# Kernel tuning notes

Hardware: AMD Instinct MI355X
Metric: run time of the kernel (lower is better)

## Reference

```python
import jax, jax.numpy as jnp
import numpy as np

VOCAB, D, H, L, SEQ = 32000, 768, 12, 6, 1024
HD = D // H
DFF = 4 * D
EPS = 1e-5


def _ln(x, g, b):
    mu = jnp.mean(x, axis=-1, keepdims=True)
    var = jnp.var(x, axis=-1, keepdims=True)
    return (x - mu) * jax.lax.rsqrt(var + EPS) * g + b


def setup_inputs() -> dict:
    key = jax.random.key(0)
    ks = jax.random.split(key, 10)
    s = lambda *sh: 0.02
    return {
        "idx": jax.random.randint(ks[0], (2, SEQ), 0, VOCAB, dtype=jnp.int64) if jax.config.jax_enable_x64 else jax.random.randint(ks[0], (2, SEQ), 0, VOCAB, dtype=jnp.int32),
        "tok_emb": jax.random.normal(ks[1], (VOCAB, D), jnp.float32) * 0.02,
        "pos_emb": jax.random.normal(ks[2], (SEQ, D), jnp.float32) * 0.02,
        "Wqkv": jax.random.normal(ks[3], (L, D, 3 * D), jnp.float32) * 0.02,
        "bqkv": jnp.zeros((L, 3 * D), jnp.float32),
        "Wo": jax.random.normal(ks[4], (L, D, D), jnp.float32) * 0.02,
        "bo": jnp.zeros((L, D), jnp.float32),
        "ln1_g": jnp.ones((L, D), jnp.float32),
        "ln1_b": jnp.zeros((L, D), jnp.float32),
        "ln2_g": jnp.ones((L, D), jnp.float32),
        "ln2_b": jnp.zeros((L, D), jnp.float32),
        "W1": jax.random.normal(ks[5], (L, D, DFF), jnp.float32) * 0.02,
        "b1": jnp.zeros((L, DFF), jnp.float32),
        "W2": jax.random.normal(ks[6], (L, DFF, D), jnp.float32) * 0.02,
        "b2": jnp.zeros((L, D), jnp.float32),
        "lnf_g": jnp.ones((D,), jnp.float32),
        "lnf_b": jnp.zeros((D,), jnp.float32),
        "Wlm": jax.random.normal(ks[7], (D, VOCAB), jnp.float32) * 0.02,
    }


def _forward(idx, tok_emb, pos_emb, Wqkv, bqkv, Wo, bo, ln1_g, ln1_b,
             ln2_g, ln2_b, W1, b1, W2, b2, lnf_g, lnf_b, Wlm):
    B, T = idx.shape
    x = tok_emb[idx] + pos_emb[None, :T]  # [B,T,D]
    causal = jnp.tril(jnp.ones((T, T), bool))  # [T,T]
    for l in range(L):
        h = _ln(x, ln1_g[l], ln1_b[l])
        qkv = h @ Wqkv[l] + bqkv[l]  # [B,T,3D]
        qkv = qkv.reshape(B, T, 3, H, HD).transpose(2, 0, 3, 1, 4)
        q, k, v = qkv[0], qkv[1], qkv[2]  # each [B,H,T,HD]
        att = jnp.einsum('bhqd,bhkd->bhqk', q, k) / np.sqrt(HD).astype(np.float32)
        att = jnp.where(causal, att, -jnp.inf)
        att = jax.nn.softmax(att, axis=-1)
        o = jnp.einsum('bhqk,bhkd->bhqd', att, v)
        o = o.transpose(0, 2, 1, 3).reshape(B, T, D)
        x = x + o @ Wo[l] + bo[l]
        h = _ln(x, ln2_g[l], ln2_b[l])
        x = x + jax.nn.gelu(h @ W1[l] + b1[l], approximate=False) @ W2[l] + b2[l]
    x = _ln(x, lnf_g, lnf_b)
    return x @ Wlm  # [B,T,VOCAB]


def reference(idx, tok_emb, pos_emb, Wqkv, bqkv, Wo, bo, ln1_g, ln1_b,
              ln2_g, ln2_b, W1, b1, W2, b2, lnf_g, lnf_b, Wlm):
    return _forward(idx, tok_emb, pos_emb, Wqkv, bqkv, Wo, bo, ln1_g, ln1_b,
                    ln2_g, ln2_b, W1, b1, W2, b2, lnf_g, lnf_b, Wlm)
```

## Files before the change

kernel.cpp:

```cpp
#include <hip/hip_runtime.h>
#include <math.h>

#define TT   1024
#define DD   768
#define HH   12
#define LLAY 6
#define DFFN 3072
#define BB   2
#define NTOK (BB*TT)

typedef __bf16 bf16;
typedef __attribute__((ext_vector_type(8))) __bf16 bf16x8;
typedef __attribute__((ext_vector_type(4))) __bf16 bf16x4;
typedef __attribute__((ext_vector_type(4))) float f32x4;

__device__ inline unsigned pack_bf16x2(float a, float b) {
    union { bf16 h[2]; unsigned u; } un;
    un.h[0] = (bf16)a; un.h[1] = (bf16)b;
    return un.u;
}

__device__ inline void gload16(const bf16* g, bf16* l) {
    __builtin_amdgcn_global_load_lds((const void*)g, (void*)l, 16, 0, 0);
}

template<int N> __device__ inline void waitcnt_vm() {
    if constexpr (N == 0) asm volatile("s_waitcnt vmcnt(0)" ::: "memory");
    else if constexpr (N == 3) asm volatile("s_waitcnt vmcnt(3)" ::: "memory");
    else if constexpr (N == 4) asm volatile("s_waitcnt vmcnt(4)" ::: "memory");
}

__global__ __launch_bounds__(256) void embed_kernel(const int* __restrict__ idx,
                                                    const float* __restrict__ tok,
                                                    const float* __restrict__ pos,
                                                    float* __restrict__ x) {
    int bt = blockIdx.x;
    int t  = bt % TT;
    int id = idx[bt];
    const float* te = tok + (size_t)id * DD;
    const float* pe = pos + (size_t)t * DD;
    float* xr = x + (size_t)bt * DD;
    for (int d = threadIdx.x; d < DD; d += 256) xr[d] = te[d] + pe[d];
}

__global__ __launch_bounds__(256) void ln_kernel(const float* __restrict__ in,
                                                 const float* __restrict__ g,
                                                 const float* __restrict__ b,
                                                 bf16* __restrict__ out) {
    const int wid = threadIdx.x >> 6, lane = threadIdx.x & 63;
    const int row = blockIdx.x * 4 + wid;
    const float* xr = in + (size_t)row * DD;
    float4 v[3];
    float s = 0.f, s2 = 0.f;
#pragma unroll
    for (int j = 0; j < 3; ++j) {
        v[j] = *(const float4*)&xr[lane * 4 + 256 * j];
        s  += v[j].x + v[j].y + v[j].z + v[j].w;
        s2 += v[j].x * v[j].x + v[j].y * v[j].y + v[j].z * v[j].z + v[j].w * v[j].w;
    }
    for (int off = 32; off; off >>= 1) { s += __shfl_down(s, off); s2 += __shfl_down(s2, off); }
    s = __shfl(s, 0); s2 = __shfl(s2, 0);
    const float mu = s / (float)DD;
    const float rs = rsqrtf(s2 / (float)DD - mu * mu + 1e-5f);
    bf16* orow = out + (size_t)row * DD;
#pragma unroll
    for (int j = 0; j < 3; ++j) {
        float4 gg = *(const float4*)&g[lane * 4 + 256 * j];
        float4 bb = *(const float4*)&b[lane * 4 + 256 * j];
        bf16x4 o;
        o[0] = (bf16)((v[j].x - mu) * rs * gg.x + bb.x);
        o[1] = (bf16)((v[j].y - mu) * rs * gg.y + bb.y);
        o[2] = (bf16)((v[j].z - mu) * rs * gg.z + bb.z);
        o[3] = (bf16)((v[j].w - mu) * rs * gg.w + bb.w);
        *(bf16x4*)&orow[lane * 4 + 256 * j] = o;
    }
}

__device__ inline void convT_tile64(const float* __restrict__ in, bf16* __restrict__ out,
                                    int K, int N, int k0, int n0) {
    __shared__ float tile[64][65];
    const int c = threadIdx.x & 63, q = threadIdx.x >> 6;
#pragma unroll
    for (int i = 0; i < 16; ++i)
        tile[q + i * 4][c] = in[(size_t)(k0 + q + i * 4) * N + n0 + c];
    __syncthreads();
#pragma unroll
    for (int i = 0; i < 16; ++i)
        out[(size_t)(n0 + q + i * 4) * K + k0 + c] = (bf16)tile[c][q + i * 4];
}

__global__ __launch_bounds__(256) void convT_kernel(const float* __restrict__ in,
                                                    bf16* __restrict__ out,
                                                    int K, int N) {
    convT_tile64(in, out, K, N, blockIdx.y * 64, blockIdx.x * 64);
}

__global__ __launch_bounds__(256) void convT4_kernel(const float* __restrict__ w0,
                                                     const float* __restrict__ w1,
                                                     const float* __restrict__ w2,
                                                     const float* __restrict__ w3,
                                                     bf16* __restrict__ o0,
                                                     bf16* __restrict__ o1,
                                                     bf16* __restrict__ o2,
                                                     bf16* __restrict__ o3) {
    int bid = blockIdx.x;
    const float* in; bf16* out; int K, N, t;
    if (bid < 432)       { in = w0; out = o0; K = 768;  N = 2304; t = bid; }
    else if (bid < 576)  { in = w1; out = o1; K = 768;  N = 768;  t = bid - 432; }
    else if (bid < 1152) { in = w2; out = o2; K = 768;  N = 3072; t = bid - 576; }
    else                 { in = w3; out = o3; K = 3072; N = 768;  t = bid - 1152; }
    int nt = N / 64;
    convT_tile64(in, out, K, N, (t / nt) * 64, (t % nt) * 64);
}

template<int BM, int EPI>
__global__ __launch_bounds__(256) void mgemm(const bf16* __restrict__ A,
                                             const bf16* __restrict__ Bt,
                                             const float* __restrict__ bias,
                                             const float* __restrict__ res,
                                             void* __restrict__ Cout,
                                             bf16* __restrict__ vtout,
                                             int M, int N, int K) {
    constexpr int MF = BM / 32;
    constexpr int NF = 4;
    constexpr int AIT = BM / 64;
    constexpr int STG = AIT + 2;
    constexpr int ASZ = BM * 32;
    constexpr int BUFE = ASZ + 128 * 32;
    __shared__ __align__(16) bf16 smem[3 * BUFE];
    int bm = blockIdx.y * BM;
    int bn = blockIdx.x * 128;
    int tid = threadIdx.x;
    int lane = tid & 63;
    int w = tid >> 6;
    int wr = w >> 1, wc = w & 1;
    int l15 = lane & 15, g = lane >> 4;

    f32x4 acc[MF][NF];
#pragma unroll
    for (int m = 0; m < MF; ++m)
#pragma unroll
        for (int n = 0; n < NF; ++n) acc[m][n] = (f32x4){0.f, 0.f, 0.f, 0.f};

    int r = lane >> 2;
    int koff = ((lane & 3) ^ ((r >> 1) & 3)) * 8;
    const bf16* Ab = A + (size_t)(bm + w * 16 + r) * K + koff;
    const bf16* Bb = Bt + (size_t)(bn + w * 16 + r) * K + koff;

    auto stage = [&](int p, int k0) {
        bf16* base = smem + p * BUFE;
        bf16* Asb = base + w * 16 * 32;
        bf16* Bsb = base + ASZ + w * 16 * 32;
#pragma unroll
        for (int it = 0; it < AIT; ++it)
            gload16(Ab + (size_t)(it * 64) * K + k0, Asb + it * 64 * 32);
#pragma unroll
        for (int it = 0; it < 2; ++it)
            gload16(Bb + (size_t)(it * 64) * K + k0, Bsb + it * 64 * 32);
    };

    stage(0, 0);
    stage(1, 32);
    waitcnt_vm<STG>();
    __builtin_amdgcn_s_barrier();
    int cur = 0;

    for (int k0 = 0; k0 < K; k0 += 32) {
        const bf16* Ac = smem + cur * BUFE;
        const bf16* Bc = Ac + ASZ;
        bf16x8 af[MF], bfv[NF];
#pragma unroll
        for (int m = 0; m < MF; ++m) {
            int row = wr * (BM / 2) + m * 16 + l15;
            int gs = g ^ ((row >> 1) & 3);
            af[m] = *(const bf16x8*)&Ac[row * 32 + gs * 8];
        }
#pragma unroll
        for (int n = 0; n < NF; ++n) {
            int row = wc * 64 + n * 16 + l15;
            int gs = g ^ ((row >> 1) & 3);
            bfv[n] = *(const bf16x8*)&Bc[row * 32 + gs * 8];
        }
        bool st = (k0 + 64 < K);
        if (st) {
            int nxt = cur + 2; if (nxt >= 3) nxt -= 3;
            stage(nxt, k0 + 64);
        }
#pragma unroll
        for (int m = 0; m < MF; ++m)
#pragma unroll
            for (int n = 0; n < NF; ++n)
                acc[m][n] = __builtin_amdgcn_mfma_f32_16x16x32_bf16(af[m], bfv[n], acc[m][n], 0, 0, 0);
        if (st) waitcnt_vm<STG>();
        else    waitcnt_vm<0>();
        __builtin_amdgcn_s_barrier();
        cur = (cur == 2) ? 0 : cur + 1;
    }

    int lq = g * 4;
#pragma unroll
    for (int m = 0; m < MF; ++m) {
#pragma unroll
        for (int n = 0; n < NF; ++n) {
            int col = bn + wc * 64 + n * 16 + l15;
            float bv = bias[col];
            if (EPI == 4 && col >= 2 * DD) {
                int row0 = bm + wr * (BM / 2) + m * 16 + lq;
                int b = row0 >> 10, t0 = row0 & 1023;
                int hd = col - 2 * DD;
                union { bf16 h[4]; unsigned long long u; } pk;
#pragma unroll
                for (int j = 0; j < 4; ++j) pk.h[j] = (bf16)(acc[m][n][j] + bv);
                *(unsigned long long*)&vtout[((size_t)(b * DD + hd)) * TT + t0] = pk.u;
            } else {
#pragma unroll
                for (int j = 0; j < 4; ++j) {
                    int row = bm + wr * (BM / 2) + m * 16 + lq + j;
                    float v = acc[m][n][j] + bv;
                    if (EPI == 2) {
                        ((float*)Cout)[(size_t)row * N + col] = v + res[(size_t)row * N + col];
                    } else if (EPI == 3) {
                        v = 0.5f * v * (1.f + erff(v * 0.70710678118654752f));
                        ((bf16*)Cout)[(size_t)row * N + col] = (bf16)v;
                    } else if (EPI == 1) {
                        ((bf16*)Cout)[(size_t)row * N + col] = (bf16)v;
                    } else {
                        if (col < DD) v *= 0.125f;
                        ((bf16*)Cout)[(size_t)row * N + col] = (bf16)v;
                    }
                }
            }
        }
    }
}

__global__ __launch_bounds__(512, 2) void lmgemm(const bf16* __restrict__ A,
                                                 const bf16* __restrict__ Bt,
                                                 float* __restrict__ C) {
    constexpr int BUFE = 2 * 256 * 64;
    __shared__ __align__(16) bf16 smem[2 * BUFE];
    const int orig = blockIdx.x;
    const int xcd = orig & 7, local = orig >> 3;
    const int bnb = xcd * 16 + (local >> 3);
    if (bnb >= 125) return;
    const int bm = (local & 7) * 256;
    const int bn = bnb * 256;
    const int tid = threadIdx.x;
    const int w = tid >> 6, lane = tid & 63;
    const int wm = w >> 2, wn = w & 3;
    const int l15 = lane & 15, g = lane >> 4;

    const int swzr = (l15 >> 1) & 7;
    const int pc0 = (g ^ swzr) * 8;

    const int r8 = lane >> 3, c8 = lane & 7;
    const bf16* agp[4]; const bf16* bgp[4];
    int aldso[4], bldso[4];
#pragma unroll
    for (int j = 0; j < 4; ++j) {
        int br = w * 32 + j * 8 + r8;
        int swz = (br >> 1) & 7;
        agp[j] = A  + (size_t)(bm + br) * DD + (c8 ^ swz) * 8;
        bgp[j] = Bt + (size_t)(bn + br) * DD + (c8 ^ swz) * 8;
        aldso[j] = (w * 32 + j * 8) * 64;
        bldso[j] = 256 * 64 + (w * 32 + j * 8) * 64;
    }

    f32x4 acc[8][4];
#pragma unroll
    for (int m = 0; m < 8; ++m)
#pragma unroll
        for (int n = 0; n < 4; ++n) acc[m][n] = (f32x4){0.f, 0.f, 0.f, 0.f};

    {
        bf16* base = smem;
#pragma unroll
        for (int j = 0; j < 4; ++j) gload16(agp[j], base + aldso[j]);
#pragma unroll
        for (int j = 0; j < 4; ++j) gload16(bgp[j], base + bldso[j]);
    }
    __syncthreads();
    int cur = 0;

    for (int t = 0; t < 12; ++t) {
        const bf16* Ar = smem + cur * BUFE;
        const bf16* Br = Ar + 256 * 64;
        bf16* nbase = smem + (cur ^ 1) * BUFE;
        const int k0n = (t + 1) * 64;
        const bool st = (t < 11);
        if (st) {
#pragma unroll
            for (int j = 0; j < 4; ++j) gload16(agp[j] + k0n, nbase + aldso[j]);
        }
        bf16x8 af[8], bfv[4];
#pragma unroll
        for (int m = 0; m < 8; ++m)
            af[m] = *(const bf16x8*)&Ar[(wm * 128 + m * 16 + l15) * 64 + pc0];
#pragma unroll
        for (int n = 0; n < 4; ++n)
            bfv[n] = *(const bf16x8*)&Br[(wn * 64 + n * 16 + l15) * 64 + pc0];
        __builtin_amdgcn_s_setprio(1);
#pragma unroll
        for (int m = 0; m < 8; ++m)
#pragma unroll
            for (int n = 0; n < 4; ++n)
                acc[m][n] = __builtin_amdgcn_mfma_f32_16x16x32_bf16(af[m], bfv[n], acc[m][n], 0, 0, 0);
        __builtin_amdgcn_s_setprio(0);
        if (st) {
#pragma unroll
            for (int j = 0; j < 4; ++j) gload16(bgp[j] + k0n, nbase + bldso[j]);
        }
#pragma unroll
        for (int m = 0; m < 8; ++m)
            af[m] = *(const bf16x8*)&Ar[(wm * 128 + m * 16 + l15) * 64 + (pc0 ^ 32)];
#pragma unroll
        for (int n = 0; n < 4; ++n)
            bfv[n] = *(const bf16x8*)&Br[(wn * 64 + n * 16 + l15) * 64 + (pc0 ^ 32)];
        __builtin_amdgcn_s_setprio(1);
#pragma unroll
        for (int m = 0; m < 8; ++m)
#pragma unroll
            for (int n = 0; n < 4; ++n)
                acc[m][n] = __builtin_amdgcn_mfma_f32_16x16x32_bf16(af[m], bfv[n], acc[m][n], 0, 0, 0);
        __builtin_amdgcn_s_setprio(0);
        __syncthreads();
        cur ^= 1;
    }

    float* eb = (float*)smem + w * (16 * 68);
    const int rr = lane >> 2, c0 = (lane & 3) * 16;
#pragma unroll
    for (int mf = 0; mf < 8; ++mf) {
#pragma unroll
        for (int n = 0; n < 4; ++n)
#pragma unroll
            for (int j = 0; j < 4; ++j)
                eb[(g * 4 + j) * 68 + n * 16 + l15] = acc[mf][n][j];
        __syncthreads();
        const float* src = &eb[rr * 68 + c0];
        float* dst = C + (size_t)(bm + wm * 128 + mf * 16 + rr) * 32000 + bn + wn * 64 + c0;
        *(float4*)(dst + 0)  = *(const float4*)(src + 0);
        *(float4*)(dst + 4)  = *(const float4*)(src + 4);
        *(float4*)(dst + 8)  = *(const float4*)(src + 8);
        *(float4*)(dst + 12) = *(const float4*)(src + 12);
        __syncthreads();
    }
}

__global__ __launch_bounds__(256) void fattn_kernel(const bf16* __restrict__ qkv,
                                                    const bf16* __restrict__ vt,
                                                    bf16* __restrict__ o) {
    const int bh = blockIdx.y;
    const int b = bh / HH, h = bh % HH;
    const int qc = gridDim.x - 1 - blockIdx.x;
    const int q0 = qc * 64;
    const int tid = threadIdx.x;
    const int w = tid >> 6, lane = tid & 63;
    const int l15 = lane & 15, g = lane >> 4;

    __shared__ __align__(16) bf16 Ks[64 * 64];
    __shared__ __align__(16) bf16 Vs[64 * 64];
    __shared__ __align__(16) bf16 Ps[4][16 * 64];

    const size_t basebt = (size_t)b * TT;
    const int qw = q0 + w * 16;
    const int qg = qw + l15;

    bf16x8 bq0, bq1;
    {
        const bf16* qp = qkv + (basebt + qw + l15) * 2304 + h * 64 + g * 8;
        bq0 = *(const bf16x8*)(qp);
        bq1 = *(const bf16x8*)(qp + 32);
    }

    float mstate = -1e30f, lstate = 0.f;
    f32x4 oacc[4];
#pragma unroll
    for (int nf = 0; nf < 4; ++nf) oacc[nf] = (f32x4){0.f, 0.f, 0.f, 0.f};

    const int swzA = (l15 & 7) << 4;
    char* const psBase = (char*)&Ps[w][0];

    const int nchunk = qc + 1;
    for (int c = 0; c < nchunk; ++c) {
        const int kc = c * 64;
        __syncthreads();
        {
            int r0 = tid >> 3;
            int e0 = (tid & 7) * 8;
#pragma unroll
            for (int i = 0; i < 2; ++i) {
                int r = r0 + 32 * i;
                int swzW = (r & 7) << 4;
                bf16x8 kv = *(const bf16x8*)&qkv[(basebt + kc + r) * 2304 + DD + h * 64 + e0];
                *(bf16x8*)((char*)Ks + r * 128 + ((e0 * 2) ^ swzW)) = kv;
                bf16x8 vv = *(const bf16x8*)&vt[((size_t)bh * 64 + r) * TT + kc + e0];
                *(bf16x8*)((char*)Vs + r * 128 + ((e0 * 2) ^ swzW)) = vv;
            }
        }
        __syncthreads();
        if (kc > qw + 15) continue;

        f32x4 s[4];
        __builtin_amdgcn_s_setprio(1);
#pragma unroll
        for (int mf = 0; mf < 4; ++mf) {
            char* kr = (char*)Ks + (16 * mf + l15) * 128;
            bf16x8 ka0 = *(const bf16x8*)(kr + ((16 * g) ^ swzA));
            bf16x8 ka1 = *(const bf16x8*)(kr + ((64 + 16 * g) ^ swzA));
            f32x4 a = (f32x4){0.f, 0.f, 0.f, 0.f};
            a = __builtin_amdgcn_mfma_f32_16x16x32_bf16(ka0, bq0, a, 0, 0, 0);
            a = __builtin_amdgcn_mfma_f32_16x16x32_bf16(ka1, bq1, a, 0, 0, 0);
            s[mf] = a;
        }
        __builtin_amdgcn_s_setprio(0);
        if (kc + 63 > qw) {
#pragma unroll
            for (int mf = 0; mf < 4; ++mf)
#pragma unroll
                for (int j = 0; j < 4; ++j)
                    if (kc + 16 * mf + 4 * g + j > qg) s[mf][j] = -1e30f;
        }
        float cm = -1e30f;
#pragma unroll
        for (int mf = 0; mf < 4; ++mf)
#pragma unroll
            for (int j = 0; j < 4; ++j) cm = fmaxf(cm, s[mf][j]);
        cm = fmaxf(cm, __shfl_xor(cm, 16));
        cm = fmaxf(cm, __shfl_xor(cm, 32));
        float mnew = fmaxf(mstate, cm);
        float sc = __expf(mstate - mnew);
        mstate = mnew;
        float p[4][4];
        float psum = 0.f;
#pragma unroll
        for (int mf = 0; mf < 4; ++mf)
#pragma unroll
            for (int j = 0; j < 4; ++j) { float pv = __expf(s[mf][j] - mnew); p[mf][j] = pv; psum += pv; }
        psum += __shfl_xor(psum, 16);
        psum += __shfl_xor(psum, 32);
        lstate = lstate * sc + psum;
#pragma unroll
        for (int mf = 0; mf < 4; ++mf) {
            unsigned lo = pack_bf16x2(p[mf][0], p[mf][1]);
            unsigned hi = pack_bf16x2(p[mf][2], p[mf][3]);
            char* dst = psBase + l15 * 128 + ((32 * mf + 8 * g) ^ swzA);
            *(unsigned*)dst = lo;
            *(unsigned*)(dst + 4) = hi;
        }
        float s0 = __shfl(sc, 4 * g + 0), s1 = __shfl(sc, 4 * g + 1);
        float s2 = __shfl(sc, 4 * g + 2), s3 = __shfl(sc, 4 * g + 3);
#pragma unroll
        for (int nf = 0; nf < 4; ++nf) {
            oacc[nf][0] *= s0; oacc[nf][1] *= s1; oacc[nf][2] *= s2; oacc[nf][3] *= s3;
        }
        bf16x8 pa0 = *(const bf16x8*)(psBase + l15 * 128 + ((16 * g) ^ swzA));
        bf16x8 pa1 = *(const bf16x8*)(psBase + l15 * 128 + ((64 + 16 * g) ^ swzA));
        __builtin_amdgcn_s_setprio(1);
#pragma unroll
        for (int nf = 0; nf < 4; ++nf) {
            char* vr = (char*)Vs + (16 * nf + l15) * 128;
            bf16x8 vb0 = *(const bf16x8*)(vr + ((16 * g) ^ swzA));
            bf16x8 vb1 = *(const bf16x8*)(vr + ((64 + 16 * g) ^ swzA));
            oacc[nf] = __builtin_amdgcn_mfma_f32_16x16x32_bf16(pa0, vb0, oacc[nf], 0, 0, 0);
            oacc[nf] = __builtin_amdgcn_mfma_f32_16x16x32_bf16(pa1, vb1, oacc[nf], 0, 0, 0);
        }
        __builtin_amdgcn_s_setprio(0);
    }
    float linv = 1.f / lstate;
    float l0 = __shfl(linv, 4 * g + 0), l1 = __shfl(linv, 4 * g + 1);
    float l2 = __shfl(linv, 4 * g + 2), l3 = __shfl(linv, 4 * g + 3);
    float lj[4] = {l0, l1, l2, l3};
#pragma unroll
    for (int j = 0; j < 4; ++j) {
        bf16* orow = o + (size_t)(basebt + qw + 4 * g + j) * DD + h * 64 + l15;
#pragma unroll
        for (int nf = 0; nf < 4; ++nf)
            orow[16 * nf] = (bf16)(oacc[nf][j] * lj[j]);
    }
}

extern "C" void kernel_launch(void* const* d_in, const int* in_sizes, int n_in,
                              void* d_out, int out_size, void* d_ws, size_t ws_size,
                              hipStream_t stream) {
    (void)in_sizes; (void)n_in; (void)out_size; (void)ws_size;
    const int*   idx  = (const int*)d_in[0];
    const float* tok  = (const float*)d_in[1];
    const float* pos  = (const float*)d_in[2];
    const float* Wqkv = (const float*)d_in[3];
    const float* bqkv = (const float*)d_in[4];
    const float* Wo   = (const float*)d_in[5];
    const float* bo   = (const float*)d_in[6];
    const float* ln1g = (const float*)d_in[7];
    const float* ln1b = (const float*)d_in[8];
    const float* ln2g = (const float*)d_in[9];
    const float* ln2b = (const float*)d_in[10];
    const float* W1   = (const float*)d_in[11];
    const float* b1   = (const float*)d_in[12];
    const float* W2   = (const float*)d_in[13];
    const float* b2   = (const float*)d_in[14];
    const float* lnfg = (const float*)d_in[15];
    const float* lnfb = (const float*)d_in[16];
    const float* Wlm  = (const float*)d_in[17];
    float* out = (float*)d_out;

    char* ws = (char*)d_ws;
    float* x     = (float*)(ws);
    bf16*  abuf0 = (bf16*)(ws + 6291456);
    bf16*  abuf1 = (bf16*)(ws + 9437184);
    bf16*  qkvb  = (bf16*)(ws + 22020096);
    bf16*  vtb   = (bf16*)(ws + 31457280);
    bf16*  wbuf  = (bf16*)(ws + 34603008);

    bf16* wq = wbuf;
    bf16* wo = wbuf + 1769472;
    bf16* w1 = wbuf + 2359296;
    bf16* w2 = wbuf + 4718592;

    embed_kernel<<<NTOK, 256, 0, stream>>>(idx, tok, pos, x);

    for (int l = 0; l < LLAY; ++l) {
        convT4_kernel<<<1728, 256, 0, stream>>>(
            Wqkv + (size_t)l * DD * 3 * DD, Wo + (size_t)l * DD * DD,
            W1 + (size_t)l * DD * DFFN, W2 + (size_t)l * DFFN * DD,
            wq, wo, w1, w2);
        ln_kernel<<<NTOK / 4, 256, 0, stream>>>(x, ln1g + l * DD, ln1b + l * DD, abuf0);
        mgemm<128, 4><<<dim3(3 * DD / 128, NTOK / 128), 256, 0, stream>>>(
            abuf0, wq, bqkv + (size_t)l * 3 * DD, nullptr, qkvb, vtb, NTOK, 3 * DD, DD);
        fattn_kernel<<<dim3(TT / 64, BB * HH), 256, 0, stream>>>(qkvb, vtb, abuf0);
        mgemm<64, 2><<<dim3(DD / 128, NTOK / 64), 256, 0, stream>>>(
            abuf0, wo, bo + (size_t)l * DD, x, x, nullptr, NTOK, DD, DD);
        ln_kernel<<<NTOK / 4, 256, 0, stream>>>(x, ln2g + l * DD, ln2b + l * DD, abuf0);
        mgemm<128, 3><<<dim3(DFFN / 128, NTOK / 128), 256, 0, stream>>>(
            abuf0, w1, b1 + (size_t)l * DFFN, nullptr, abuf1, nullptr, NTOK, DFFN, DD);
        mgemm<64, 2><<<dim3(DD / 128, NTOK / 64), 256, 0, stream>>>(
            abuf1, w2, b2 + (size_t)l * DD, x, x, nullptr, NTOK, DD, DFFN);
    }
    ln_kernel<<<NTOK / 4, 256, 0, stream>>>(x, lnfg, lnfb, abuf0);
    convT_kernel<<<dim3(32000 / 64, DD / 64), 256, 0, stream>>>(Wlm, wbuf, DD, 32000);
    lmgemm<<<1024, 512, 0, stream>>>(abuf0, wbuf, out);
}
```

Baseline: 995.1 us.

## Prefetch K/V tiles into registers in attention; relax LM-head epilogue sync

The flash attention loop now loads the next K/V chunk from global memory into registers while the current chunk is computed, then writes it to shared memory at the top of the next iteration. This hides global load latency behind the MFMA and softmax work. Separately, the LM-head GEMM epilogue replaces its two block-wide barriers per fragment with a per-wave LDS wait and uses nontemporal float4 stores for the large logits output. This is safe because each wave uses its own staging region, and it cuts barrier stalls and cache pollution on the 256MB write, at the cost of some extra registers in the attention kernel.

New measurement: 1.271 ms. 27.8% more time.

```diff
diff --git a/kernel.cpp b/kernel.cpp
--- a/kernel.cpp
+++ b/kernel.cpp
@@ -336,14 +336,17 @@
 #pragma unroll
             for (int j = 0; j < 4; ++j)
                 eb[(g * 4 + j) * 68 + n * 16 + l15] = acc[mf][n][j];
-        __syncthreads();
+        asm volatile("s_waitcnt lgkmcnt(0)" ::: "memory");
         const float* src = &eb[rr * 68 + c0];
         float* dst = C + (size_t)(bm + wm * 128 + mf * 16 + rr) * 32000 + bn + wn * 64 + c0;
-        *(float4*)(dst + 0)  = *(const float4*)(src + 0);
-        *(float4*)(dst + 4)  = *(const float4*)(src + 4);
-        *(float4*)(dst + 8)  = *(const float4*)(src + 8);
-        *(float4*)(dst + 12) = *(const float4*)(src + 12);
-        __syncthreads();
+        f32x4 v0 = *(const f32x4*)(src + 0);
+        f32x4 v1 = *(const f32x4*)(src + 4);
+        f32x4 v2 = *(const f32x4*)(src + 8);
+        f32x4 v3 = *(const f32x4*)(src + 12);
+        __builtin_nontemporal_store(v0, (f32x4*)(dst + 0));
+        __builtin_nontemporal_store(v1, (f32x4*)(dst + 4));
+        __builtin_nontemporal_store(v2, (f32x4*)(dst + 8));
+        __builtin_nontemporal_store(v3, (f32x4*)(dst + 12));
     }
 }
 
@@ -381,91 +384,104 @@
     const int swzA = (l15 & 7) << 4;
     char* const psBase = (char*)&Ps[w][0];
 
+    const int r0 = tid >> 3;
+    const int e0 = (tid & 7) * 8;
+    bf16x8 kreg[2], vreg[2];
+#pragma unroll
+    for (int i = 0; i < 2; ++i) {
+        int r = r0 + 32 * i;
+        kreg[i] = *(const bf16x8*)&qkv[(basebt + r) * 2304 + DD + h * 64 + e0];
+        vreg[i] = *(const bf16x8*)&vt[((size_t)bh * 64 + r) * TT + e0];
+    }
+
     const int nchunk = qc + 1;
     for (int c = 0; c < nchunk; ++c) {
         const int kc = c * 64;
+#pragma unroll
+        for (int i = 0; i < 2; ++i) {
+            int r = r0 + 32 * i;
+            int swzW = (r & 7) << 4;
+            *(bf16x8*)((char*)Ks + r * 128 + ((e0 * 2) ^ swzW)) = kreg[i];
+            *(bf16x8*)((char*)Vs + r * 128 + ((e0 * 2) ^ swzW)) = vreg[i];
+        }
         __syncthreads();
-        {
-            int r0 = tid >> 3;
-            int e0 = (tid & 7) * 8;
+        if (c + 1 < nchunk) {
+            const int kc2 = kc + 64;
 #pragma unroll
             for (int i = 0; i < 2; ++i) {
                 int r = r0 + 32 * i;
-                int swzW = (r & 7) << 4;
-                bf16x8 kv = *(const bf16x8*)&qkv[(basebt + kc + r) * 2304 + DD + h * 64 + e0];
-                *(bf16x8*)((char*)Ks + r * 128 + ((e0 * 2) ^ swzW)) = kv;
-                bf16x8 vv = *(const bf16x8*)&vt[((size_t)bh * 64 + r) * TT + kc + e0];
-                *(bf16x8*)((char*)Vs + r * 128 + ((e0 * 2) ^ swzW)) = vv;
-            }
+                kreg[i] = *(const bf16x8*)&qkv[(basebt + kc2 + r) * 2304 + DD + h * 64 + e0];
+                vreg[i] = *(const bf16x8*)&vt[((size_t)bh * 64 + r) * TT + kc2 + e0];
+            }
+        }
+        if (kc <= qw + 15) {
+            f32x4 s[4];
+            __builtin_amdgcn_s_setprio(1);
+#pragma unroll
+            for (int mf = 0; mf < 4; ++mf) {
+                char* kr = (char*)Ks + (16 * mf + l15) * 128;
+                bf16x8 ka0 = *(const bf16x8*)(kr + ((16 * g) ^ swzA));
+                bf16x8 ka1 = *(const bf16x8*)(kr + ((64 + 16 * g) ^ swzA));
+                f32x4 a = (f32x4){0.f, 0.f, 0.f, 0.f};
+                a = __builtin_amdgcn_mfma_f32_16x16x32_bf16(ka0, bq0, a, 0, 0, 0);
+                a = __builtin_amdgcn_mfma_f32_16x16x32_bf16(ka1, bq1, a, 0, 0, 0);
+                s[mf] = a;
+            }
+            __builtin_amdgcn_s_setprio(0);
+            if (kc + 63 > qw) {
+#pragma unroll
+                for (int mf = 0; mf < 4; ++mf)
+#pragma unroll
+                    for (int j = 0; j < 4; ++j)
+                        if (kc + 16 * mf + 4 * g + j > qg) s[mf][j] = -1e30f;
+            }
+            float cm = -1e30f;
+#pragma unroll
+            for (int mf = 0; mf < 4; ++mf)
+#pragma unroll
+                for (int j = 0; j < 4; ++j) cm = fmaxf(cm, s[mf][j]);
+            cm = fmaxf(cm, __shfl_xor(cm, 16));
+            cm = fmaxf(cm, __shfl_xor(cm, 32));
+            float mnew = fmaxf(mstate, cm);
+            float sc = __expf(mstate - mnew);
+            mstate = mnew;
+            float p[4][4];
+            float psum = 0.f;
+#pragma unroll
+            for (int mf = 0; mf < 4; ++mf)
+#pragma unroll
+                for (int j = 0; j < 4; ++j) { float pv = __expf(s[mf][j] - mnew); p[mf][j] = pv; psum += pv; }
+            psum += __shfl_xor(psum, 16);
+            psum += __shfl_xor(psum, 32);
+            lstate = lstate * sc + psum;
+#pragma unroll
+            for (int mf = 0; mf < 4; ++mf) {
+                unsigned lo = pack_bf16x2(p[mf][0], p[mf][1]);
+                unsigned hi = pack_bf16x2(p[mf][2], p[mf][3]);
+                char* dst = psBase + l15 * 128 + ((32 * mf + 8 * g) ^ swzA);
+                *(unsigned*)dst = lo;
+                *(unsigned*)(dst + 4) = hi;
+            }
+            float s0 = __shfl(sc, 4 * g + 0), s1 = __shfl(sc, 4 * g + 1);
+            float s2 = __shfl(sc, 4 * g + 2), s3 = __shfl(sc, 4 * g + 3);
+#pragma unroll
+            for (int nf = 0; nf < 4; ++nf) {
+                oacc[nf][0] *= s0; oacc[nf][1] *= s1; oacc[nf][2] *= s2; oacc[nf][3] *= s3;
+            }
+            bf16x8 pa0 = *(const bf16x8*)(psBase + l15 * 128 + ((16 * g) ^ swzA));
+            bf16x8 pa1 = *(const bf16x8*)(psBase + l15 * 128 + ((64 + 16 * g) ^ swzA));
+            __builtin_amdgcn_s_setprio(1);
+#pragma unroll
+            for (int nf = 0; nf < 4; ++nf) {
+                char* vr = (char*)Vs + (16 * nf + l15) * 128;
+                bf16x8 vb0 = *(const bf16x8*)(vr + ((16 * g) ^ swzA));
+                bf16x8 vb1 = *(const bf16x8*)(vr + ((64 + 16 * g) ^ swzA));
+                oacc[nf] = __builtin_amdgcn_mfma_f32_16x16x32_bf16(pa0, vb0, oacc[nf], 0, 0, 0);
+                oacc[nf] = __builtin_amdgcn_mfma_f32_16x16x32_bf16(pa1, vb1, oacc[nf], 0, 0, 0);
+            }
+            __builtin_amdgcn_s_setprio(0);
         }
         __syncthreads();
-        if (kc > qw + 15) continue;
-
-        f32x4 s[4];
-        __builtin_amdgcn_s_setprio(1);
-#pragma unroll
-        for (int mf = 0; mf < 4; ++mf) {
-            char* kr = (char*)Ks + (16 * mf + l15) * 128;
-            bf16x8 ka0 = *(const bf16x8*)(kr + ((16 * g) ^ swzA));
-            bf16x8 ka1 = *(const bf16x8*)(kr + ((64 + 16 * g) ^ swzA));
-            f32x4 a = (f32x4){0.f, 0.f, 0.f, 0.f};
-            a = __builtin_amdgcn_mfma_f32_16x16x32_bf16(ka0, bq0, a, 0, 0, 0);
-            a = __builtin_amdgcn_mfma_f32_16x16x32_bf16(ka1, bq1, a, 0, 0, 0);
-            s[mf] = a;
-        }
-        __builtin_amdgcn_s_setprio(0);
-        if (kc + 63 > qw) {
-#pragma unroll
-            for (int mf = 0; mf < 4; ++mf)
-#pragma unroll
-                for (int j = 0; j < 4; ++j)
-                    if (kc + 16 * mf + 4 * g + j > qg) s[mf][j] = -1e30f;
-        }
-        float cm = -1e30f;
-#pragma unroll
-        for (int mf = 0; mf < 4; ++mf)
-#pragma unroll
-            for (int j = 0; j < 4; ++j) cm = fmaxf(cm, s[mf][j]);
-        cm = fmaxf(cm, __shfl_xor(cm, 16));
-        cm = fmaxf(cm, __shfl_xor(cm, 32));
-        float mnew = fmaxf(mstate, cm);
-        float sc = __expf(mstate - mnew);
-        mstate = mnew;
-        float p[4][4];
-        float psum = 0.f;
-#pragma unroll
-        for (int mf = 0; mf < 4; ++mf)
-#pragma unroll
-            for (int j = 0; j < 4; ++j) { float pv = __expf(s[mf][j] - mnew); p[mf][j] = pv; psum += pv; }
-        psum += __shfl_xor(psum, 16);
-        psum += __shfl_xor(psum, 32);
-        lstate = lstate * sc + psum;
-#pragma unroll
-        for (int mf = 0; mf < 4; ++mf) {
-            unsigned lo = pack_bf16x2(p[mf][0], p[mf][1]);
-            unsigned hi = pack_bf16x2(p[mf][2], p[mf][3]);
-            char* dst = psBase + l15 * 128 + ((32 * mf + 8 * g) ^ swzA);
-            *(unsigned*)dst = lo;
-            *(unsigned*)(dst + 4) = hi;
-        }
-        float s0 = __shfl(sc, 4 * g + 0), s1 = __shfl(sc, 4 * g + 1);
-        float s2 = __shfl(sc, 4 * g + 2), s3 = __shfl(sc, 4 * g + 3);
-#pragma unroll
-        for (int nf = 0; nf < 4; ++nf) {
-            oacc[nf][0] *= s0; oacc[nf][1] *= s1; oacc[nf][2] *= s2; oacc[nf][3] *= s3;
-        }
-        bf16x8 pa0 = *(const bf16x8*)(psBase + l15 * 128 + ((16 * g) ^ swzA));
-        bf16x8 pa1 = *(const bf16x8*)(psBase + l15 * 128 + ((64 + 16 * g) ^ swzA));
-        __builtin_amdgcn_s_setprio(1);
-#pragma unroll
-        for (int nf = 0; nf < 4; ++nf) {
-            char* vr = (char*)Vs + (16 * nf + l15) * 128;
-            bf16x8 vb0 = *(const bf16x8*)(vr + ((16 * g) ^ swzA));
-            bf16x8 vb1 = *(const bf16x8*)(vr + ((64 + 16 * g) ^ swzA));
-            oacc[nf] = __builtin_amdgcn_mfma_f32_16x16x32_bf16(pa0, vb0, oacc[nf], 0, 0, 0);
-            oacc[nf] = __builtin_amdgcn_mfma_f32_16x16x32_bf16(pa1, vb1, oacc[nf], 0, 0, 0);
-        }
-        __builtin_amdgcn_s_setprio(0);
     }
     float linv = 1.f / lstate;
     float l0 = __shfl(linv, 4 * g + 0), l1 = __shfl(linv, 4 * g + 1);
```
